# Kernel optimization log

Measured on AMD Instinct MI355X. Metric: run time of the kernel, lower is better.

The kernel has to match this reference:

```python
import jax, jax.numpy as jnp
import numpy as np

NS, NT, DF, H, O = 200000, 50000, 20, 64, 64
NE, NL = 1000000, 500000


def setup_inputs() -> dict:
    key = jax.random.key(0)
    ks = jax.random.split(key, 24)
    inp = {
        'target_x': jax.random.normal(ks[0], (NT, DF), jnp.float32),
        'source_node_id': jnp.arange(NS, dtype=jnp.int64),
        'target_node_id': jnp.arange(NT, dtype=jnp.int64),
        'edge_src': jax.random.randint(ks[1], (NE,), 0, NS),
        'edge_dst': jax.random.randint(ks[2], (NE,), 0, NT),
        'label_src': jax.random.randint(ks[3], (NL,), 0, NS),
        'label_dst': jax.random.randint(ks[4], (NL,), 0, NT),
        'src_emb': jax.random.normal(ks[5], (NS, H), jnp.float32) * 0.05,
        'tgt_emb': jax.random.normal(ks[6], (NT, H), jnp.float32) * 0.05,
        'lin_W': jax.random.normal(ks[7], (DF, H), jnp.float32) * 0.05,
        'lin_b': jnp.zeros((H,), jnp.float32),
    }
    # SAGEConv params: (Wl, bl, Wr) per edge type per layer. st = source->target, ts = target->source
    dims = {'st1': (H, H), 'ts1': (H, H), 'st2': (H, O), 'ts2': (H, O)}
    i = 8
    for name, (din, dout) in dims.items():
        inp['Wl_' + name] = jax.random.normal(ks[i], (din, dout), jnp.float32) * 0.05
        inp['bl_' + name] = jnp.zeros((dout,), jnp.float32)
        inp['Wr_' + name] = jax.random.normal(ks[i + 1], (din, dout), jnp.float32) * 0.05
        i += 2
    return inp


def _sage(x_src, x_dst, src_idx, dst_idx, n_dst, Wl, bl, Wr):
    # PyG SAGEConv, aggr='mean': lin_l(mean_{j in N(i)} x_j) + lin_r(x_i)
    msg = x_src[src_idx]                                   # [E, d] gather
    agg = jax.ops.segment_sum(msg, dst_idx, num_segments=n_dst)
    deg = jax.ops.segment_sum(jnp.ones((src_idx.shape[0],), x_src.dtype), dst_idx, num_segments=n_dst)
    mean = agg / jnp.maximum(deg, 1.0)[:, None]
    return mean @ Wl + bl + x_dst @ Wr


def reference(target_x, source_node_id, target_node_id, edge_src, edge_dst,
              label_src, label_dst, src_emb, tgt_emb, lin_W, lin_b,
              Wl_st1, bl_st1, Wr_st1, Wl_ts1, bl_ts1, Wr_ts1,
              Wl_st2, bl_st2, Wr_st2, Wl_ts2, bl_ts2, Wr_ts2):
    ns, nt = src_emb.shape[0], tgt_emb.shape[0]
    x_s = src_emb[source_node_id]                          # [NS, H]
    x_t = target_x @ lin_W + lin_b + tgt_emb[target_node_id]  # [NT, H]
    # layer 1 (per edge type, summed per dst type; each dst type has one incoming type)
    h_t = _sage(x_s, x_t, edge_src, edge_dst, nt, Wl_st1, bl_st1, Wr_st1)
    h_s = _sage(x_t, x_s, edge_dst, edge_src, ns, Wl_ts1, bl_ts1, Wr_ts1)
    h_t, h_s = jax.nn.relu(h_t), jax.nn.relu(h_s)
    # layer 2
    o_t = _sage(h_s, h_t, edge_src, edge_dst, nt, Wl_st2, bl_st2, Wr_st2)
    o_s = _sage(h_t, h_s, edge_dst, edge_src, ns, Wl_ts2, bl_ts2, Wr_ts2)
    # dot-product link classifier
    return (o_s[label_src] * o_t[label_dst]).sum(axis=-1)  # [NL]
```

## Files before the change

kernel.cpp:

```cpp
#include <hip/hip_runtime.h>

#define NSRC 200000
#define NTGT 50000
#define DF   20
#define HD   64
#define NE   1000000
#define NL   500000

#define SH_T 6
#define SH_S 8
#define NB   782
#define CHUNK 8192
#define NCH  ((NE + CHUNK - 1) / CHUNK)

typedef unsigned short ushort_t;
typedef short s16x8 __attribute__((ext_vector_type(8)));
typedef float f32x4 __attribute__((ext_vector_type(4)));

__device__ __forceinline__ float bf2f(ushort_t u) {
    return __uint_as_float(((unsigned)u) << 16);
}
__device__ __forceinline__ ushort_t f2bf(float f) {
    unsigned u = __float_as_uint(f);
    return (ushort_t)((u + 0x7fffu + ((u >> 16) & 1u)) >> 16);
}

__global__ __launch_bounds__(1024) void chunk_hist(
    const int* __restrict__ es, const int* __restrict__ ed, int ne,
    int* __restrict__ cnt_t, int* __restrict__ cnt_s)
{
    __shared__ int h[NB];
    const int dir  = blockIdx.y;
    const int c    = blockIdx.x;
    const int base = c * CHUNK;
    const int n    = min(CHUNK, ne - base);
    const int* key = dir ? es : ed;
    const int sh   = dir ? SH_S : SH_T;
    int* cnt       = dir ? cnt_s : cnt_t;

    for (int i = threadIdx.x; i < NB; i += 1024) h[i] = 0;
    __syncthreads();
    for (int i = threadIdx.x; i < n; i += 1024)
        atomicAdd(&h[key[base + i] >> sh], 1);
    __syncthreads();
    for (int i = threadIdx.x; i < NB; i += 1024) cnt[c * NB + i] = h[i];
}

__global__ __launch_bounds__(1024) void chunk_scan(
    int* __restrict__ cnt_t, int* __restrict__ cnt_s,
    int* __restrict__ bt_t, int* __restrict__ bt_s)
{
    int* cnt = blockIdx.x ? cnt_s : cnt_t;
    int* bt  = blockIdx.x ? bt_s  : bt_t;
    const int b = threadIdx.x;
    if (b < NB) {
        int run = 0;
        for (int c = 0; c < NCH; ++c) {
            int v = cnt[c * NB + b];
            cnt[c * NB + b] = run;
            run += v;
        }
        bt[b] = run;
    }
}

__global__ __launch_bounds__(1024) void bucket_scan(
    const int* __restrict__ bt_t, int* __restrict__ bb_t,
    const int* __restrict__ bt_s, int* __restrict__ bb_s)
{
    const int* bt = blockIdx.x ? bt_s : bt_t;
    int* bb       = blockIdx.x ? bb_s : bb_t;

    __shared__ int s[1024];
    const int tid = threadIdx.x;
    int v = (tid < NB) ? bt[tid] : 0;
    s[tid] = v;
    __syncthreads();
    for (int d = 1; d < 1024; d <<= 1) {
        int t = (tid >= d) ? s[tid - d] : 0;
        __syncthreads();
        s[tid] += t;
        __syncthreads();
    }
    int incl = s[tid];
    if (tid < NB) bb[tid] = incl - v;
    if (tid == NB - 1) bb[NB] = incl;
}

__global__ __launch_bounds__(1024) void bin_fill2(
    const int* __restrict__ es, const int* __restrict__ ed, int ne,
    const int* __restrict__ cnt_t, const int* __restrict__ cnt_s,
    const int* __restrict__ bb_t, const int* __restrict__ bb_s,
    int2* __restrict__ pairs_t, int2* __restrict__ pairs_s)
{
    __shared__ int cur[NB];
    const int dir  = blockIdx.y;
    const int c    = blockIdx.x;
    const int base = c * CHUNK;
    const int n    = min(CHUNK, ne - base);
    const int* key = dir ? es : ed;
    const int* oth = dir ? ed : es;
    const int sh   = dir ? SH_S : SH_T;
    const int* cnt = dir ? cnt_s : cnt_t;
    const int* bb  = dir ? bb_s  : bb_t;
    int2* pairs    = dir ? pairs_s : pairs_t;

    for (int i = threadIdx.x; i < NB; i += 1024)
        cur[i] = bb[i] + cnt[c * NB + i];
    __syncthreads();
    for (int i = threadIdx.x; i < n; i += 1024) {
        int k = key[base + i], o = oth[base + i];
        int p = atomicAdd(&cur[k >> sh], 1);
        pairs[p] = make_int2(o, k);
    }
}

template <int SHIFT>
__global__ __launch_bounds__(256) void bucket_build(
    const int2* __restrict__ pairs, const int* __restrict__ bb,
    int* __restrict__ rp, int* __restrict__ col, int n, int ne)
{
    __shared__ int hist[256];
    __shared__ int scn[256];
    __shared__ int cur[256];
    const int b = blockIdx.x;
    const int tid = threadIdx.x;
    const int beg = bb[b], end = bb[b + 1];
    const int row0 = b << SHIFT;

    hist[tid] = 0;
    __syncthreads();
    for (int e = beg + tid; e < end; e += 256)
        atomicAdd(&hist[pairs[e].y - row0], 1);
    __syncthreads();

    int v = hist[tid];
    scn[tid] = v;
    __syncthreads();
    for (int d = 1; d < 256; d <<= 1) {
        int t = (tid >= d) ? scn[tid - d] : 0;
        __syncthreads();
        scn[tid] += t;
        __syncthreads();
    }
    int ex = scn[tid] - v;
    cur[tid] = ex;
    int row = row0 + tid;
    if (tid < (1 << SHIFT) && row < n) rp[row] = beg + ex;
    if (b == 0 && tid == 0) rp[n] = ne;
    __syncthreads();

    for (int e = beg + tid; e < end; e += 256) {
        int2 pr = pairs[e];
        int p = atomicAdd(&cur[pr.y - row0], 1);
        col[beg + p] = pr.x;
    }
}

__global__ void compute_xt(const float* __restrict__ tx, const float* __restrict__ W,
                           const float* __restrict__ b, const float* __restrict__ temb,
                           ushort_t* __restrict__ xb)
{
    int stride = gridDim.x * blockDim.x;
    for (int i = blockIdx.x * blockDim.x + threadIdx.x; i < NTGT * HD; i += stride) {
        int n = i >> 6, k = i & 63;
        float acc = b[k] + temb[i];
#pragma unroll
        for (int d = 0; d < DF; ++d) acc += tx[n * DF + d] * W[d * HD + k];
        xb[i] = f2bf(acc);
    }
}

__global__ void to_bf16(const float* __restrict__ in, ushort_t* __restrict__ out, int n)
{
    int stride = gridDim.x * blockDim.x;
    for (int i = blockIdx.x * blockDim.x + threadIdx.x; i < n; i += stride)
        out[i] = f2bf(in[i]);
}

__global__ void pack_weights(
    const float* __restrict__ Wl0, const float* __restrict__ Wr0,
    const float* __restrict__ Wl1, const float* __restrict__ Wr1,
    const float* __restrict__ Wl2, const float* __restrict__ Wr2,
    const float* __restrict__ Wl3, const float* __restrict__ Wr3,
    ushort_t* __restrict__ wt)
{
    int i = blockIdx.x * blockDim.x + threadIdx.x;
    if (i >= 4 * 64 * 128) return;
    int set = i >> 13, rem = i & 8191;
    int j = rem >> 7, k = rem & 127;
    const float* Wl = set == 0 ? Wl0 : set == 1 ? Wl1 : set == 2 ? Wl2 : Wl3;
    const float* Wr = set == 0 ? Wr0 : set == 1 ? Wr1 : set == 2 ? Wr2 : Wr3;
    float v = (k < 64) ? Wl[k * 64 + j] : Wr[(k - 64) * 64 + j];
    wt[i] = f2bf(v);
}

__global__ __launch_bounds__(256) void aggregate_o(
    const ushort_t* __restrict__ table, const int* __restrict__ rp,
    const int* __restrict__ col, ushort_t* __restrict__ mean, int n_dst)
{
    const int el = threadIdx.x & 7;
    const int ew = threadIdx.x >> 3;
    const int d0 = el * 8;
    const int stride = gridDim.x * 32;

    for (int node = blockIdx.x * 32 + ew; node < n_dst; node += stride) {
        const int beg = rp[node], end = rp[node + 1];
        float a0[8], a1[8], a2[8], a3[8];
#pragma unroll
        for (int i = 0; i < 8; ++i) { a0[i] = 0.f; a1[i] = 0.f; a2[i] = 0.f; a3[i] = 0.f; }
        int e = beg;
        for (; e + 4 <= end; e += 4) {
            int c0 = col[e], c1 = col[e + 1], c2 = col[e + 2], c3 = col[e + 3];
            s16x8 v0 = *(const s16x8*)&table[(size_t)c0 * HD + d0];
            s16x8 v1 = *(const s16x8*)&table[(size_t)c1 * HD + d0];
            s16x8 v2 = *(const s16x8*)&table[(size_t)c2 * HD + d0];
            s16x8 v3 = *(const s16x8*)&table[(size_t)c3 * HD + d0];
#pragma unroll
            for (int i = 0; i < 8; ++i) {
                a0[i] += bf2f((ushort_t)v0[i]);
                a1[i] += bf2f((ushort_t)v1[i]);
                a2[i] += bf2f((ushort_t)v2[i]);
                a3[i] += bf2f((ushort_t)v3[i]);
            }
        }
        for (; e < end; ++e) {
            s16x8 v = *(const s16x8*)&table[(size_t)col[e] * HD + d0];
#pragma unroll
            for (int i = 0; i < 8; ++i) a0[i] += bf2f((ushort_t)v[i]);
        }
        float degf = (float)(end - beg);
        float inv  = degf > 0.f ? 1.f / degf : 0.f;
        s16x8 o;
#pragma unroll
        for (int i = 0; i < 8; ++i)
            o[i] = (short)f2bf((a0[i] + a1[i] + a2[i] + a3[i]) * inv);
        *(s16x8*)&mean[(size_t)node * HD + d0] = o;
    }
}

template <bool RELU>
__global__ __launch_bounds__(256) void transform_m(
    const ushort_t* __restrict__ mean, const ushort_t* __restrict__ xd,
    const ushort_t* __restrict__ wt,
    const float* __restrict__ bl, ushort_t* __restrict__ out, int n)
{
    const int lane = threadIdx.x & 63;
    const int wid  = threadIdx.x >> 6;
    const int lr   = lane & 15;
    const int kg   = lane >> 4;

    s16x8 b[4][4];
#pragma unroll
    for (int jb = 0; jb < 4; ++jb)
#pragma unroll
        for (int kb = 0; kb < 4; ++kb)
            b[jb][kb] = *(const s16x8*)&wt[(jb * 16 + lr) * 128 + kb * 32 + kg * 8];

    float bias[4];
#pragma unroll
    for (int jb = 0; jb < 4; ++jb) bias[jb] = bl[jb * 16 + lr];

    const int ntiles = (n + 63) >> 6;
    for (int tile = blockIdx.x; tile < ntiles; tile += gridDim.x) {
        const int arow = tile * 64 + wid * 16 + lr;
        s16x8 a[4];
        if (arow < n) {
            const ushort_t* mrow = mean + (size_t)arow * HD;
            const ushort_t* xrow = xd   + (size_t)arow * HD;
            a[0] = *(const s16x8*)(mrow + kg * 8);
            a[1] = *(const s16x8*)(mrow + 32 + kg * 8);
            a[2] = *(const s16x8*)(xrow + kg * 8);
            a[3] = *(const s16x8*)(xrow + 32 + kg * 8);
        } else {
            s16x8 z = {0, 0, 0, 0, 0, 0, 0, 0};
            a[0] = z; a[1] = z; a[2] = z; a[3] = z;
        }

        const int drow0 = tile * 64 + wid * 16 + kg * 4;
#pragma unroll
        for (int jb = 0; jb < 4; ++jb) {
            f32x4 acc = {bias[jb], bias[jb], bias[jb], bias[jb]};
#pragma unroll
            for (int kb = 0; kb < 4; ++kb)
                acc = __builtin_amdgcn_mfma_f32_16x16x32_bf16(a[kb], b[jb][kb], acc, 0, 0, 0);
#pragma unroll
            for (int r = 0; r < 4; ++r) {
                int nn = drow0 + r;
                if (nn < n) {
                    float v = acc[r];
                    if (RELU) v = fmaxf(v, 0.f);
                    out[(size_t)nn * HD + jb * 16 + lr] = f2bf(v);
                }
            }
        }
    }
}

__global__ __launch_bounds__(256) void classify_b(
    const ushort_t* __restrict__ os, const ushort_t* __restrict__ ot,
    const int* __restrict__ ls, const int* __restrict__ lt,
    float* __restrict__ out, int nl)
{
    const int lane = threadIdx.x & 63;
    const int sub  = lane >> 4;
    const int g    = (lane & 15) * 4;
    int w = (blockIdx.x * blockDim.x + threadIdx.x) >> 6;
    const int wstride = (gridDim.x * blockDim.x) >> 6;

    for (int l0 = w * 8; l0 < nl; l0 += wstride * 8) {
        int la = l0 + sub;
        int lb = l0 + 4 + sub;
        float pa = 0.f, pb = 0.f;
        if (la < nl) {
            int a = ls[la], b = lt[la];
            ushort4 va = *(const ushort4*)&os[(size_t)a * HD + g];
            ushort4 vb = *(const ushort4*)&ot[(size_t)b * HD + g];
            pa = bf2f(va.x) * bf2f(vb.x) + bf2f(va.y) * bf2f(vb.y)
               + bf2f(va.z) * bf2f(vb.z) + bf2f(va.w) * bf2f(vb.w);
        }
        if (lb < nl) {
            int a = ls[lb], b = lt[lb];
            ushort4 va = *(const ushort4*)&os[(size_t)a * HD + g];
            ushort4 vb = *(const ushort4*)&ot[(size_t)b * HD + g];
            pb = bf2f(va.x) * bf2f(vb.x) + bf2f(va.y) * bf2f(vb.y)
               + bf2f(va.z) * bf2f(vb.z) + bf2f(va.w) * bf2f(vb.w);
        }
#pragma unroll
        for (int o = 8; o > 0; o >>= 1) {
            pa += __shfl_xor(pa, o, 64);
            pb += __shfl_xor(pb, o, 64);
        }
        if ((lane & 15) == 0) {
            if (la < nl) out[la] = pa;
            if (lb < nl) out[lb] = pb;
        }
    }
}

extern "C" void kernel_launch(void* const* d_in, const int* in_sizes, int n_in,
                              void* d_out, int out_size, void* d_ws, size_t ws_size,
                              hipStream_t stream)
{
    const float* target_x = (const float*)d_in[0];
    const int* edge_src  = (const int*)d_in[3];
    const int* edge_dst  = (const int*)d_in[4];
    const int* label_src = (const int*)d_in[5];
    const int* label_dst = (const int*)d_in[6];
    const float* src_emb = (const float*)d_in[7];
    const float* tgt_emb = (const float*)d_in[8];
    const float* lin_W   = (const float*)d_in[9];
    const float* lin_b   = (const float*)d_in[10];
    const float* Wl_st1 = (const float*)d_in[11];
    const float* bl_st1 = (const float*)d_in[12];
    const float* Wr_st1 = (const float*)d_in[13];
    const float* Wl_ts1 = (const float*)d_in[14];
    const float* bl_ts1 = (const float*)d_in[15];
    const float* Wr_ts1 = (const float*)d_in[16];
    const float* Wl_st2 = (const float*)d_in[17];
    const float* bl_st2 = (const float*)d_in[18];
    const float* Wr_st2 = (const float*)d_in[19];
    const float* Wl_ts2 = (const float*)d_in[20];
    const float* bl_ts2 = (const float*)d_in[21];
    const float* Wr_ts2 = (const float*)d_in[22];
    float* out = (float*)d_out;

    char* ws = (char*)d_ws;
    size_t off = 0;
    auto take = [&](size_t bytes) -> char* {
        char* p = ws + off;
        off = (off + bytes + 255) & ~(size_t)255;
        return p;
    };
    int* cnt_t = (int*)take((size_t)NCH * NB * 4);
    int* cnt_s = (int*)take((size_t)NCH * NB * 4);
    int* bt_t  = (int*)take((size_t)NB * 4);
    int* bt_s  = (int*)take((size_t)NB * 4);
    int* bb_t  = (int*)take((size_t)(NB + 1) * 4);
    int* bb_s  = (int*)take((size_t)(NB + 1) * 4);
    int* rp_t  = (int*)take((size_t)(NTGT + 1) * 4);
    int* rp_s  = (int*)take((size_t)(NSRC + 1) * 4);
    int* col_t = (int*)take((size_t)NE * 4);
    int* col_s = (int*)take((size_t)NE * 4);
    ushort_t* wt   = (ushort_t*)take((size_t)4 * 64 * 128 * 2);
    ushort_t* xb_t = (ushort_t*)take((size_t)NTGT * HD * 2);
    ushort_t* sb   = (ushort_t*)take((size_t)NSRC * HD * 2);
    ushort_t* hb_t = (ushort_t*)take((size_t)NTGT * HD * 2);
    ushort_t* hb_s = (ushort_t*)take((size_t)NSRC * HD * 2);
    ushort_t* mb_t = (ushort_t*)take((size_t)NTGT * HD * 2);
    ushort_t* mb_s = (ushort_t*)take((size_t)NSRC * HD * 2);
    ushort_t* ob_t = mb_t;
    ushort_t* ob_s = mb_s;
    int2* pairs_t = (int2*)mb_s;
    int2* pairs_s = pairs_t + NE;

    dim3 gch(NCH, 2);
    chunk_hist<<<gch, 1024, 0, stream>>>(edge_src, edge_dst, NE, cnt_t, cnt_s);
    chunk_scan<<<2, 1024, 0, stream>>>(cnt_t, cnt_s, bt_t, bt_s);
    bucket_scan<<<2, 1024, 0, stream>>>(bt_t, bb_t, bt_s, bb_s);
    bin_fill2<<<gch, 1024, 0, stream>>>(edge_src, edge_dst, NE,
                                        cnt_t, cnt_s, bb_t, bb_s, pairs_t, pairs_s);
    bucket_build<SH_T><<<NB, 256, 0, stream>>>(pairs_t, bb_t, rp_t, col_t, NTGT, NE);
    bucket_build<SH_S><<<NB, 256, 0, stream>>>(pairs_s, bb_s, rp_s, col_s, NSRC, NE);

    pack_weights<<<128, 256, 0, stream>>>(Wl_st1, Wr_st1, Wl_ts1, Wr_ts1,
                                          Wl_st2, Wr_st2, Wl_ts2, Wr_ts2, wt);
    compute_xt<<<2048, 256, 0, stream>>>(target_x, lin_W, lin_b, tgt_emb, xb_t);
    to_bf16<<<2048, 256, 0, stream>>>(src_emb, sb, NSRC * HD);

    aggregate_o<<<2048, 256, 0, stream>>>(sb,   rp_t, col_t, mb_t, NTGT);
    aggregate_o<<<2048, 256, 0, stream>>>(xb_t, rp_s, col_s, mb_s, NSRC);
    transform_m<true><<<782, 256, 0, stream>>>(mb_t, xb_t, wt + 0 * 8192, bl_st1, hb_t, NTGT);
    transform_m<true><<<3125, 256, 0, stream>>>(mb_s, sb, wt + 1 * 8192, bl_ts1, hb_s, NSRC);

    aggregate_o<<<2048, 256, 0, stream>>>(hb_s, rp_t, col_t, mb_t, NTGT);
    aggregate_o<<<2048, 256, 0, stream>>>(hb_t, rp_s, col_s, mb_s, NSRC);
    transform_m<false><<<782, 256, 0, stream>>>(mb_t, hb_t, wt + 2 * 8192, bl_st2, ob_t, NTGT);
    transform_m<false><<<3125, 256, 0, stream>>>(mb_s, hb_s, wt + 3 * 8192, bl_ts2, ob_s, NSRC);

    classify_b<<<2048, 256, 0, stream>>>(ob_s, ob_t, label_src, label_dst, out, NL);
}
```

Measured before the change: 312.4 us.

## Fuse neighbor mean aggregation with MFMA transform per 64-node tile

Merges the aggregate and transform kernels into one sage_tile kernel. Each block gathers neighbor means for 64 nodes into shared memory, then runs the bf16 MFMA transform on that tile, so the mean buffers no longer go through global memory. It also folds compute_xt and to_bf16 into one prep kernel. The cost is that weight fragments are reloaded once per tile block instead of once per persistent block, there is one grid per layer sized to the tile count, and separate workspace is needed for the pairs and output buffers.

```diff
diff --git a/kernel.cpp b/kernel.cpp
--- a/kernel.cpp
+++ b/kernel.cpp
@@ -157,25 +157,21 @@
     }
 }
 
-__global__ void compute_xt(const float* __restrict__ tx, const float* __restrict__ W,
-                           const float* __restrict__ b, const float* __restrict__ temb,
-                           ushort_t* __restrict__ xb)
+__global__ void prep_features(const float* __restrict__ tx, const float* __restrict__ W,
+                              const float* __restrict__ b, const float* __restrict__ temb,
+                              const float* __restrict__ semb,
+                              ushort_t* __restrict__ xb, ushort_t* __restrict__ sb)
 {
     int stride = gridDim.x * blockDim.x;
-    for (int i = blockIdx.x * blockDim.x + threadIdx.x; i < NTGT * HD; i += stride) {
+    int id = blockIdx.x * blockDim.x + threadIdx.x;
+    for (int i = id; i < NTGT * HD; i += stride) {
         int n = i >> 6, k = i & 63;
         float acc = b[k] + temb[i];
 #pragma unroll
         for (int d = 0; d < DF; ++d) acc += tx[n * DF + d] * W[d * HD + k];
         xb[i] = f2bf(acc);
     }
-}
-
-__global__ void to_bf16(const float* __restrict__ in, ushort_t* __restrict__ out, int n)
-{
-    int stride = gridDim.x * blockDim.x;
-    for (int i = blockIdx.x * blockDim.x + threadIdx.x; i < n; i += stride)
-        out[i] = f2bf(in[i]);
+    for (int i = id; i < NSRC * HD; i += stride) sb[i] = f2bf(semb[i]);
 }
 
 __global__ void pack_weights(
@@ -195,58 +191,62 @@
     wt[i] = f2bf(v);
 }
 
-__global__ __launch_bounds__(256) void aggregate_o(
+template <bool RELU>
+__global__ __launch_bounds__(256) void sage_tile(
     const ushort_t* __restrict__ table, const int* __restrict__ rp,
-    const int* __restrict__ col, ushort_t* __restrict__ mean, int n_dst)
-{
-    const int el = threadIdx.x & 7;
-    const int ew = threadIdx.x >> 3;
-    const int d0 = el * 8;
-    const int stride = gridDim.x * 32;
-
-    for (int node = blockIdx.x * 32 + ew; node < n_dst; node += stride) {
-        const int beg = rp[node], end = rp[node + 1];
-        float a0[8], a1[8], a2[8], a3[8];
-#pragma unroll
-        for (int i = 0; i < 8; ++i) { a0[i] = 0.f; a1[i] = 0.f; a2[i] = 0.f; a3[i] = 0.f; }
-        int e = beg;
-        for (; e + 4 <= end; e += 4) {
-            int c0 = col[e], c1 = col[e + 1], c2 = col[e + 2], c3 = col[e + 3];
-            s16x8 v0 = *(const s16x8*)&table[(size_t)c0 * HD + d0];
-            s16x8 v1 = *(const s16x8*)&table[(size_t)c1 * HD + d0];
-            s16x8 v2 = *(const s16x8*)&table[(size_t)c2 * HD + d0];
-            s16x8 v3 = *(const s16x8*)&table[(size_t)c3 * HD + d0];
-#pragma unroll
-            for (int i = 0; i < 8; ++i) {
-                a0[i] += bf2f((ushort_t)v0[i]);
-                a1[i] += bf2f((ushort_t)v1[i]);
-                a2[i] += bf2f((ushort_t)v2[i]);
-                a3[i] += bf2f((ushort_t)v3[i]);
+    const int* __restrict__ col, const ushort_t* __restrict__ xd,
+    const ushort_t* __restrict__ wt, const float* __restrict__ bl,
+    ushort_t* __restrict__ out, int n)
+{
+    __shared__ ushort_t smean[64][72];
+    const int tid  = threadIdx.x;
+    const int el   = tid & 7;
+    const int ew   = tid >> 3;
+    const int d0   = el * 8;
+    const int base = blockIdx.x * 64;
+
+#pragma unroll
+    for (int half = 0; half < 2; ++half) {
+        const int row  = ew + half * 32;
+        const int node = base + row;
+        s16x8 o = {0, 0, 0, 0, 0, 0, 0, 0};
+        if (node < n) {
+            const int beg = rp[node], end = rp[node + 1];
+            float a0[8], a1[8], a2[8], a3[8];
+#pragma unroll
+            for (int i = 0; i < 8; ++i) { a0[i] = 0.f; a1[i] = 0.f; a2[i] = 0.f; a3[i] = 0.f; }
+            int e = beg;
+            for (; e + 4 <= end; e += 4) {
+                int c0 = col[e], c1 = col[e + 1], c2 = col[e + 2], c3 = col[e + 3];
+                s16x8 v0 = *(const s16x8*)&table[(size_t)c0 * HD + d0];
+                s16x8 v1 = *(const s16x8*)&table[(size_t)c1 * HD + d0];
+                s16x8 v2 = *(const s16x8*)&table[(size_t)c2 * HD + d0];
+                s16x8 v3 = *(const s16x8*)&table[(size_t)c3 * HD + d0];
+#pragma unroll
+                for (int i = 0; i < 8; ++i) {
+                    a0[i] += bf2f((ushort_t)v0[i]);
+                    a1[i] += bf2f((ushort_t)v1[i]);
+                    a2[i] += bf2f((ushort_t)v2[i]);
+                    a3[i] += bf2f((ushort_t)v3[i]);
+                }
             }
-        }
-        for (; e < end; ++e) {
-            s16x8 v = *(const s16x8*)&table[(size_t)col[e] * HD + d0];
-#pragma unroll
-            for (int i = 0; i < 8; ++i) a0[i] += bf2f((ushort_t)v[i]);
-        }
-        float degf = (float)(end - beg);
-        float inv  = degf > 0.f ? 1.f / degf : 0.f;
-        s16x8 o;
-#pragma unroll
-        for (int i = 0; i < 8; ++i)
-            o[i] = (short)f2bf((a0[i] + a1[i] + a2[i] + a3[i]) * inv);
-        *(s16x8*)&mean[(size_t)node * HD + d0] = o;
-    }
-}
-
-template <bool RELU>
-__global__ __launch_bounds__(256) void transform_m(
-    const ushort_t* __restrict__ mean, const ushort_t* __restrict__ xd,
-    const ushort_t* __restrict__ wt,
-    const float* __restrict__ bl, ushort_t* __restrict__ out, int n)
-{
-    const int lane = threadIdx.x & 63;
-    const int wid  = threadIdx.x >> 6;
+            for (; e < end; ++e) {
+                s16x8 v = *(const s16x8*)&table[(size_t)col[e] * HD + d0];
+#pragma unroll
+                for (int i = 0; i < 8; ++i) a0[i] += bf2f((ushort_t)v[i]);
+            }
+            float degf = (float)(end - beg);
+            float inv  = degf > 0.f ? 1.f / degf : 0.f;
+#pragma unroll
+            for (int i = 0; i < 8; ++i)
+                o[i] = (short)f2bf((a0[i] + a1[i] + a2[i] + a3[i]) * inv);
+        }
+        *(s16x8*)&smean[row][d0] = o;
+    }
+    __syncthreads();
+
+    const int lane = tid & 63;
+    const int wid  = tid >> 6;
     const int lr   = lane & 15;
     const int kg   = lane >> 4;
 
@@ -261,37 +261,33 @@
 #pragma unroll
     for (int jb = 0; jb < 4; ++jb) bias[jb] = bl[jb * 16 + lr];
 
-    const int ntiles = (n + 63) >> 6;
-    for (int tile = blockIdx.x; tile < ntiles; tile += gridDim.x) {
-        const int arow = tile * 64 + wid * 16 + lr;
-        s16x8 a[4];
-        if (arow < n) {
-            const ushort_t* mrow = mean + (size_t)arow * HD;
-            const ushort_t* xrow = xd   + (size_t)arow * HD;
-            a[0] = *(const s16x8*)(mrow + kg * 8);
-            a[1] = *(const s16x8*)(mrow + 32 + kg * 8);
-            a[2] = *(const s16x8*)(xrow + kg * 8);
-            a[3] = *(const s16x8*)(xrow + 32 + kg * 8);
-        } else {
-            s16x8 z = {0, 0, 0, 0, 0, 0, 0, 0};
-            a[0] = z; a[1] = z; a[2] = z; a[3] = z;
-        }
-
-        const int drow0 = tile * 64 + wid * 16 + kg * 4;
-#pragma unroll
-        for (int jb = 0; jb < 4; ++jb) {
-            f32x4 acc = {bias[jb], bias[jb], bias[jb], bias[jb]};
-#pragma unroll
-            for (int kb = 0; kb < 4; ++kb)
-                acc = __builtin_amdgcn_mfma_f32_16x16x32_bf16(a[kb], b[jb][kb], acc, 0, 0, 0);
-#pragma unroll
-            for (int r = 0; r < 4; ++r) {
-                int nn = drow0 + r;
-                if (nn < n) {
-                    float v = acc[r];
-                    if (RELU) v = fmaxf(v, 0.f);
-                    out[(size_t)nn * HD + jb * 16 + lr] = f2bf(v);
-                }
+    const int arow = base + wid * 16 + lr;
+    s16x8 a[4];
+    a[0] = *(const s16x8*)&smean[wid * 16 + lr][kg * 8];
+    a[1] = *(const s16x8*)&smean[wid * 16 + lr][32 + kg * 8];
+    if (arow < n) {
+        const ushort_t* xrow = xd + (size_t)arow * HD;
+        a[2] = *(const s16x8*)(xrow + kg * 8);
+        a[3] = *(const s16x8*)(xrow + 32 + kg * 8);
+    } else {
+        s16x8 z = {0, 0, 0, 0, 0, 0, 0, 0};
+        a[2] = z; a[3] = z;
+    }
+
+    const int drow0 = base + wid * 16 + kg * 4;
+#pragma unroll
+    for (int jb = 0; jb < 4; ++jb) {
+        f32x4 acc = {bias[jb], bias[jb], bias[jb], bias[jb]};
+#pragma unroll
+        for (int kb = 0; kb < 4; ++kb)
+            acc = __builtin_amdgcn_mfma_f32_16x16x32_bf16(a[kb], b[jb][kb], acc, 0, 0, 0);
+#pragma unroll
+        for (int r = 0; r < 4; ++r) {
+            int nn = drow0 + r;
+            if (nn < n) {
+                float v = acc[r];
+                if (RELU) v = fmaxf(v, 0.f);
+                out[(size_t)nn * HD + jb * 16 + lr] = f2bf(v);
             }
         }
     }
@@ -382,17 +378,15 @@
     int* rp_s  = (int*)take((size_t)(NSRC + 1) * 4);
     int* col_t = (int*)take((size_t)NE * 4);
     int* col_s = (int*)take((size_t)NE * 4);
+    int2* pairs_t = (int2*)take((size_t)NE * 8);
+    int2* pairs_s = (int2*)take((size_t)NE * 8);
     ushort_t* wt   = (ushort_t*)take((size_t)4 * 64 * 128 * 2);
     ushort_t* xb_t = (ushort_t*)take((size_t)NTGT * HD * 2);
     ushort_t* sb   = (ushort_t*)take((size_t)NSRC * HD * 2);
     ushort_t* hb_t = (ushort_t*)take((size_t)NTGT * HD * 2);
     ushort_t* hb_s = (ushort_t*)take((size_t)NSRC * HD * 2);
-    ushort_t* mb_t = (ushort_t*)take((size_t)NTGT * HD * 2);
-    ushort_t* mb_s = (ushort_t*)take((size_t)NSRC * HD * 2);
-    ushort_t* ob_t = mb_t;
-    ushort_t* ob_s = mb_s;
-    int2* pairs_t = (int2*)mb_s;
-    int2* pairs_s = pairs_t + NE;
+    ushort_t* ob_t = (ushort_t*)take((size_t)NTGT * HD * 2);
+    ushort_t* ob_s = (ushort_t*)take((size_t)NSRC * HD * 2);
 
     dim3 gch(NCH, 2);
     chunk_hist<<<gch, 1024, 0, stream>>>(edge_src, edge_dst, NE, cnt_t, cnt_s);
@@ -405,18 +399,20 @@
 
     pack_weights<<<128, 256, 0, stream>>>(Wl_st1, Wr_st1, Wl_ts1, Wr_ts1,
                                           Wl_st2, Wr_st2, Wl_ts2, Wr_ts2, wt);
-    compute_xt<<<2048, 256, 0, stream>>>(target_x, lin_W, lin_b, tgt_emb, xb_t);
-    to_bf16<<<2048, 256, 0, stream>>>(src_emb, sb, NSRC * HD);
-
-    aggregate_o<<<2048, 256, 0, stream>>>(sb,   rp_t, col_t, mb_t, NTGT);
-    aggregate_o<<<2048, 256, 0, stream>>>(xb_t, rp_s, col_s, mb_s, NSRC);
-    transform_m<true><<<782, 256, 0, stream>>>(mb_t, xb_t, wt + 0 * 8192, bl_st1, hb_t, NTGT);
-    transform_m<true><<<3125, 256, 0, stream>>>(mb_s, sb, wt + 1 * 8192, bl_ts1, hb_s, NSRC);
-
-    aggregate_o<<<2048, 256, 0, stream>>>(hb_s, rp_t, col_t, mb_t, NTGT);
-    aggregate_o<<<2048, 256, 0, stream>>>(hb_t, rp_s, col_s, mb_s, NSRC);
-    transform_m<false><<<782, 256, 0, stream>>>(mb_t, hb_t, wt + 2 * 8192, bl_st2, ob_t, NTGT);
-    transform_m<false><<<3125, 256, 0, stream>>>(mb_s, hb_s, wt + 3 * 8192, bl_ts2, ob_s, NSRC);
+    prep_features<<<2048, 256, 0, stream>>>(target_x, lin_W, lin_b, tgt_emb,
+                                            src_emb, xb_t, sb);
+
+    const int GT = (NTGT + 63) / 64;
+    const int GS = (NSRC + 63) / 64;
+
+    sage_tile<true><<<GT, 256, 0, stream>>>(sb,   rp_t, col_t, xb_t,
+                                            wt + 0 * 8192, bl_st1, hb_t, NTGT);
+    sage_tile<true><<<GS, 256, 0, stream>>>(xb_t, rp_s, col_s, sb,
+                                            wt + 1 * 8192, bl_ts1, hb_s, NSRC);
+    sage_tile<false><<<GT, 256, 0, stream>>>(hb_s, rp_t, col_t, hb_t,
+                                             wt + 2 * 8192, bl_st2, ob_t, NTGT);
+    sage_tile<false><<<GS, 256, 0, stream>>>(hb_t, rp_s, col_s, hb_s,
+                                             wt + 3 * 8192, bl_ts2, ob_s, NSRC);
 
     classify_b<<<2048, 256, 0, stream>>>(ob_s, ob_t, label_src, label_dst, out, NL);
 }
```

Result: faster. 295.8 us (-5.3%).
